# Optimization experiments

Hardware: AMD Instinct MI355X
Metric: run time of the kernel (lower is better)

The kernel has to match this reference:

```python
import jax, jax.numpy as jnp
import numpy as np

N_GRID = 16      # reservoir_n
CHANNELS = 4
R = 2            # receptive-field radius -> 5x5 kernel
T_STEPS = 8
NEG_SLOPE = 0.1


def _extract_patches(S):
    # S: [b, C, n, n] -> patches [b, C, 5, 5, n, n] (kernel offsets u,v)
    Sp = jnp.pad(S, ((0, 0), (0, 0), (R, R), (R, R)))
    k = 2 * R + 1
    rows = [jnp.stack([Sp[:, :, du:du + N_GRID, dv:dv + N_GRID] for dv in range(k)], axis=2)
            for du in range(k)]
    return jnp.stack(rows, axis=2)  # [b, C, k, k, n, n]


def _reservoir_step(S, W):
    # W: [n, n, C_out, C_in, k, k]; per-pixel unique weights (locally connected)
    patches = _extract_patches(S)                       # [b, c, u, v, y, x]
    out = jnp.einsum('bcuvyx,yxocuv->boyx', patches, W)  # [b, C, n, n]
    return jnp.where(out > 0, out, NEG_SLOPE * out)      # leaky_relu(0.1)


def setup_inputs() -> dict:
    key = jax.random.key(0)
    k1, k2 = jax.random.split(key)
    x = jax.random.normal(k1, (8192, 784), dtype=jnp.float32)
    # scale weights down so the T-step recurrence stays numerically tame
    W = jax.random.normal(k2, (N_GRID, N_GRID, CHANNELS, CHANNELS, 2 * R + 1, 2 * R + 1),
                          dtype=jnp.float32) * 0.05
    return {"x": x, "W": W}


def reference(x, W):
    batch = x.shape[0]
    total = N_GRID * N_GRID * CHANNELS  # 1024
    padded = jnp.pad(x, ((0, 0), (0, total - x.shape[1])))
    S = padded.reshape(batch, CHANNELS, N_GRID, N_GRID)
    for _ in range(T_STEPS):
        S = _reservoir_step(S, W)
    S_pooled = S.mean(axis=1)                 # pool over channels -> [b, n, n]
    return S_pooled.reshape(batch, -1)        # [b, n*n]
```

## Files before the change

### kernel.cpp

```cpp
#include <hip/hip_runtime.h>

#define NG 16
#define NC 4
#define BPB 8
#define TSTEPS 8
#define PITCH 34
#define CROW (NG * PITCH)

__device__ __forceinline__ void fma8(float w, const float4& s0, const float4& s1,
                                     float4& a0, float4& a1) {
    a0.x = fmaf(w, s0.x, a0.x);
    a0.y = fmaf(w, s0.y, a0.y);
    a0.z = fmaf(w, s0.z, a0.z);
    a0.w = fmaf(w, s0.w, a0.w);
    a1.x = fmaf(w, s1.x, a1.x);
    a1.y = fmaf(w, s1.y, a1.y);
    a1.z = fmaf(w, s1.z, a1.z);
    a1.w = fmaf(w, s1.w, a1.w);
}

__device__ __forceinline__ float4 lrelu4(float4 v) {
    float4 r;
    r.x = fmaxf(v.x, 0.1f * v.x);
    r.y = fmaxf(v.y, 0.1f * v.y);
    r.z = fmaxf(v.z, 0.1f * v.z);
    r.w = fmaxf(v.w, 0.1f * v.w);
    return r;
}

template<int CTRL>
__device__ __forceinline__ float dppf(float x) {
    return __int_as_float(__builtin_amdgcn_update_dpp(
        0, __float_as_int(x), CTRL, 0xF, 0xF, true));
}
template<int CTRL>
__device__ __forceinline__ float4 dpp4(float4 v) {
    float4 r;
    r.x = dppf<CTRL>(v.x);
    r.y = dppf<CTRL>(v.y);
    r.z = dppf<CTRL>(v.z);
    r.w = dppf<CTRL>(v.w);
    return r;
}

__global__ void wt_transpose(const float* __restrict__ W, float4* __restrict__ Wt) {
    int t = blockIdx.x * 256 + threadIdx.x;
    if (t >= 25600) return;
    int r = t >> 8;
    int pix = t & 255;
    int c = r / 25, uv = r - c * 25, u = uv / 5, v = uv - u * 5;
    int y = pix >> 4, x = pix & 15;
    float4 w = make_float4(0.f, 0.f, 0.f, 0.f);
    if ((unsigned)(y + u - 2) < 16u && (unsigned)(x + v - 2) < 16u) {
        int base = pix * 400 + c * 25 + uv;
        w.x = W[base];
        w.y = W[base + 100];
        w.z = W[base + 200];
        w.w = W[base + 300];
    }
    Wt[r * 256 + pix] = w;
}

__global__ __launch_bounds__(256, 4)
__attribute__((amdgpu_waves_per_eu(4, 4)))
void reservoir_kernel(const float* __restrict__ X, const float4* __restrict__ Wt,
                      float* __restrict__ out, int batch) {
    __shared__ float4 smv[NC * CROW];
    float* smf = reinterpret_cast<float*>(smv);

    const int tid = threadIdx.x;
    const int y = tid >> 4;
    const int x = tid & 15;
    const long itemBase = (long)blockIdx.x * BPB;

    const float4* Wp = Wt + tid;

    float4 b0_0, b0_1, b0_2, b0_3, b0_4;
    float4 b1_0, b1_1, b1_2, b1_3, b1_4;

#define LOADBUF(B, OFF) \
    B##_0 = Wp[(OFF)]; \
    B##_1 = Wp[(OFF) + 256]; \
    B##_2 = Wp[(OFF) + 512]; \
    B##_3 = Wp[(OFF) + 768]; \
    B##_4 = Wp[(OFF) + 1024];

    LOADBUF(b0, 0)

    for (int b = 0; b < BPB; ++b) {
        long item = itemBase + b;
        const float* xr = X + item * 784;
        const int g = b >> 2, j = b & 3;
        #pragma unroll
        for (int kk = 0; kk < 4; ++kk) {
            int idx = tid + kk * 256;
            float v = 0.f;
            if (idx < 784 && item < batch) v = __builtin_nontemporal_load(&xr[idx]);
            int c = idx >> 8, rem = idx & 255, yy = rem >> 4, xx = rem & 15;
            int phys = g ^ ((xx >> 2) & 1);
            smf[((c * NG + yy) * PITCH + xx * 2 + phys) * 4 + j] = v;
        }
    }

    int ybf[5];
    #pragma unroll
    for (int u = 0; u < 5; ++u) {
        int yy = y + u - 2;
        yy = yy < 0 ? 0 : (yy > 15 ? 15 : yy);
        ybf[u] = yy * PITCH;
    }
    const int swx = (x >> 2) & 1;
    const int xown = x * 2 + swx;
    const int pa = y * PITCH + x * 2;

    __syncthreads();

#define CHUNK_DPP(B, CB, U) { \
    const int i0 = (CB) + ybf[U] + xown; \
    const float4 s0 = smv[i0]; \
    const float4 s1 = smv[i0 ^ 1]; \
    fma8(B##_2.x, s0, s1, a00, a01); \
    fma8(B##_2.y, s0, s1, a10, a11); \
    fma8(B##_2.z, s0, s1, a20, a21); \
    fma8(B##_2.w, s0, s1, a30, a31); \
    { const float4 t0 = dpp4<0x111>(s0), t1 = dpp4<0x111>(s1); \
      fma8(B##_1.x, t0, t1, a00, a01); \
      fma8(B##_1.y, t0, t1, a10, a11); \
      fma8(B##_1.z, t0, t1, a20, a21); \
      fma8(B##_1.w, t0, t1, a30, a31); } \
    { const float4 t0 = dpp4<0x101>(s0), t1 = dpp4<0x101>(s1); \
      fma8(B##_3.x, t0, t1, a00, a01); \
      fma8(B##_3.y, t0, t1, a10, a11); \
      fma8(B##_3.z, t0, t1, a20, a21); \
      fma8(B##_3.w, t0, t1, a30, a31); } \
    { const float4 t0 = dpp4<0x112>(s0), t1 = dpp4<0x112>(s1); \
      fma8(B##_0.x, t0, t1, a00, a01); \
      fma8(B##_0.y, t0, t1, a10, a11); \
      fma8(B##_0.z, t0, t1, a20, a21); \
      fma8(B##_0.w, t0, t1, a30, a31); } \
    { const float4 t0 = dpp4<0x102>(s0), t1 = dpp4<0x102>(s1); \
      fma8(B##_4.x, t0, t1, a00, a01); \
      fma8(B##_4.y, t0, t1, a10, a11); \
      fma8(B##_4.z, t0, t1, a20, a21); \
      fma8(B##_4.w, t0, t1, a30, a31); } }

#define CH_A(CB, U, POFF) \
    LOADBUF(b1, POFF) \
    CHUNK_DPP(b0, CB, U)
#define CH_B(CB, U, POFF) \
    LOADBUF(b0, POFF) \
    CHUNK_DPP(b1, CB, U)

    #pragma unroll 1
    for (int t = 0; t < TSTEPS; ++t) {
        float4 a00 = {0,0,0,0}, a01 = {0,0,0,0};
        float4 a10 = {0,0,0,0}, a11 = {0,0,0,0};
        float4 a20 = {0,0,0,0}, a21 = {0,0,0,0};
        float4 a30 = {0,0,0,0}, a31 = {0,0,0,0};

        #pragma unroll 1
        for (int g = 0; g < 4; g += 2) {
            const int cb0 = g * CROW;
            const int cb1 = cb0 + CROW;
            const int wo = g * 6400;
            const int wlast = (g == 2) ? 0 : wo + 12800;

            CH_A(cb0, 0, wo + 1280)
            CH_B(cb0, 1, wo + 2560)
            CH_A(cb0, 2, wo + 3840)
            CH_B(cb0, 3, wo + 5120)
            CH_A(cb0, 4, wo + 6400)
            CH_B(cb1, 0, wo + 7680)
            CH_A(cb1, 1, wo + 8960)
            CH_B(cb1, 2, wo + 10240)
            CH_A(cb1, 3, wo + 11520)
            CH_B(cb1, 4, wlast)
        }

        a00 = lrelu4(a00); a01 = lrelu4(a01);
        a10 = lrelu4(a10); a11 = lrelu4(a11);
        a20 = lrelu4(a20); a21 = lrelu4(a21);
        a30 = lrelu4(a30); a31 = lrelu4(a31);

        if (t < TSTEPS - 1) {
            __syncthreads();
            int c0 = 0 * CROW + pa;
            smv[c0 + swx] = a00; smv[c0 + (swx ^ 1)] = a01;
            int c1 = 1 * CROW + pa;
            smv[c1 + swx] = a10; smv[c1 + (swx ^ 1)] = a11;
            int c2 = 2 * CROW + pa;
            smv[c2 + swx] = a20; smv[c2 + (swx ^ 1)] = a21;
            int c3 = 3 * CROW + pa;
            smv[c3 + swx] = a30; smv[c3 + (swx ^ 1)] = a31;
            __syncthreads();
        } else {
            float4 p0, p1;
            p0.x = (a00.x + a10.x + a20.x + a30.x) * 0.25f;
            p0.y = (a00.y + a10.y + a20.y + a30.y) * 0.25f;
            p0.z = (a00.z + a10.z + a20.z + a30.z) * 0.25f;
            p0.w = (a00.w + a10.w + a20.w + a30.w) * 0.25f;
            p1.x = (a01.x + a11.x + a21.x + a31.x) * 0.25f;
            p1.y = (a01.y + a11.y + a21.y + a31.y) * 0.25f;
            p1.z = (a01.z + a11.z + a21.z + a31.z) * 0.25f;
            p1.w = (a01.w + a11.w + a21.w + a31.w) * 0.25f;
            long ob = itemBase * 256 + tid;
            if (itemBase + 0 < batch) __builtin_nontemporal_store(p0.x, &out[ob + 0 * 256]);
            if (itemBase + 1 < batch) __builtin_nontemporal_store(p0.y, &out[ob + 1 * 256]);
            if (itemBase + 2 < batch) __builtin_nontemporal_store(p0.z, &out[ob + 2 * 256]);
            if (itemBase + 3 < batch) __builtin_nontemporal_store(p0.w, &out[ob + 3 * 256]);
            if (itemBase + 4 < batch) __builtin_nontemporal_store(p1.x, &out[ob + 4 * 256]);
            if (itemBase + 5 < batch) __builtin_nontemporal_store(p1.y, &out[ob + 5 * 256]);
            if (itemBase + 6 < batch) __builtin_nontemporal_store(p1.z, &out[ob + 6 * 256]);
            if (itemBase + 7 < batch) __builtin_nontemporal_store(p1.w, &out[ob + 7 * 256]);
        }
    }
}

extern "C" void kernel_launch(void* const* d_in, const int* in_sizes, int n_in,
                              void* d_out, int out_size, void* d_ws, size_t ws_size,
                              hipStream_t stream) {
    const float* X = (const float*)d_in[0];
    const float* W = (const float*)d_in[1];
    float* out = (float*)d_out;
    const int batch = in_sizes[0] / 784;
    const int blocks = (batch + BPB - 1) / BPB;

    wt_transpose<<<100, 256, 0, stream>>>(W, (float4*)d_ws);
    reservoir_kernel<<<blocks, 256, 0, stream>>>(
        X, (const float4*)d_ws, out, batch);
}
```

Baseline: 235.8 us.

## Split each block's eight items across two 256-thread halves with loop-based weight loads

Doubles the block to 512 threads so each thread owns 4 batch items instead of 8, halving accumulator registers and raising occupancy. The fully unrolled double-buffered weight pipeline is replaced with rolled c/u loops that load the next weight set after a sched barrier. In exchange, each weight is now loaded and reused by two threads, giving half the FMA work per weight load, and prefetch overlap is weaker.

Result: slower. 266.1 us (+12.8%).

```diff
diff --git a/kernel.cpp b/kernel.cpp
--- a/kernel.cpp
+++ b/kernel.cpp
@@ -7,16 +7,11 @@
 #define PITCH 34
 #define CROW (NG * PITCH)
 
-__device__ __forceinline__ void fma8(float w, const float4& s0, const float4& s1,
-                                     float4& a0, float4& a1) {
-    a0.x = fmaf(w, s0.x, a0.x);
-    a0.y = fmaf(w, s0.y, a0.y);
-    a0.z = fmaf(w, s0.z, a0.z);
-    a0.w = fmaf(w, s0.w, a0.w);
-    a1.x = fmaf(w, s1.x, a1.x);
-    a1.y = fmaf(w, s1.y, a1.y);
-    a1.z = fmaf(w, s1.z, a1.z);
-    a1.w = fmaf(w, s1.w, a1.w);
+__device__ __forceinline__ void fma4(float w, const float4& s, float4& a) {
+    a.x = fmaf(w, s.x, a.x);
+    a.y = fmaf(w, s.y, a.y);
+    a.z = fmaf(w, s.z, a.z);
+    a.w = fmaf(w, s.w, a.w);
 }
 
 __device__ __forceinline__ float4 lrelu4(float4 v) {
@@ -61,157 +56,103 @@
     Wt[r * 256 + pix] = w;
 }
 
-__global__ __launch_bounds__(256, 4)
-__attribute__((amdgpu_waves_per_eu(4, 4)))
+__global__ __launch_bounds__(512, 8)
 void reservoir_kernel(const float* __restrict__ X, const float4* __restrict__ Wt,
                       float* __restrict__ out, int batch) {
     __shared__ float4 smv[NC * CROW];
     float* smf = reinterpret_cast<float*>(smv);
 
     const int tid = threadIdx.x;
-    const int y = tid >> 4;
-    const int x = tid & 15;
+    const int bh  = tid >> 8;
+    const int pix = tid & 255;
+    const int y = pix >> 4;
+    const int x = pix & 15;
     const long itemBase = (long)blockIdx.x * BPB;
-
-    const float4* Wp = Wt + tid;
-
-    float4 b0_0, b0_1, b0_2, b0_3, b0_4;
-    float4 b1_0, b1_1, b1_2, b1_3, b1_4;
-
-#define LOADBUF(B, OFF) \
-    B##_0 = Wp[(OFF)]; \
-    B##_1 = Wp[(OFF) + 256]; \
-    B##_2 = Wp[(OFF) + 512]; \
-    B##_3 = Wp[(OFF) + 768]; \
-    B##_4 = Wp[(OFF) + 1024];
-
-    LOADBUF(b0, 0)
 
     for (int b = 0; b < BPB; ++b) {
         long item = itemBase + b;
-        const float* xr = X + item * 784;
-        const int g = b >> 2, j = b & 3;
         #pragma unroll
-        for (int kk = 0; kk < 4; ++kk) {
-            int idx = tid + kk * 256;
+        for (int k = 0; k < 2; ++k) {
+            int idx = tid + k * 512;
             float v = 0.f;
-            if (idx < 784 && item < batch) v = __builtin_nontemporal_load(&xr[idx]);
+            if (idx < 784 && item < batch)
+                v = __builtin_nontemporal_load(&X[item * 784 + idx]);
             int c = idx >> 8, rem = idx & 255, yy = rem >> 4, xx = rem & 15;
-            int phys = g ^ ((xx >> 2) & 1);
-            smf[((c * NG + yy) * PITCH + xx * 2 + phys) * 4 + j] = v;
+            int phys = (b >> 2) ^ ((xx >> 2) & 1);
+            smf[((c * NG + yy) * PITCH + xx * 2 + phys) * 4 + (b & 3)] = v;
         }
     }
 
-    int ybf[5];
-    #pragma unroll
-    for (int u = 0; u < 5; ++u) {
-        int yy = y + u - 2;
-        yy = yy < 0 ? 0 : (yy > 15 ? 15 : yy);
-        ybf[u] = yy * PITCH;
-    }
     const int swx = (x >> 2) & 1;
-    const int xown = x * 2 + swx;
-    const int pa = y * PITCH + x * 2;
+    const int xq  = x * 2 + (bh ^ swx);
+
+    const float4* Wp = Wt + pix;
+    float4 w0 = Wp[0], w1 = Wp[256], w2 = Wp[512], w3 = Wp[768], w4 = Wp[1024];
+    int wnext = 1280;
 
     __syncthreads();
 
-#define CHUNK_DPP(B, CB, U) { \
-    const int i0 = (CB) + ybf[U] + xown; \
-    const float4 s0 = smv[i0]; \
-    const float4 s1 = smv[i0 ^ 1]; \
-    fma8(B##_2.x, s0, s1, a00, a01); \
-    fma8(B##_2.y, s0, s1, a10, a11); \
-    fma8(B##_2.z, s0, s1, a20, a21); \
-    fma8(B##_2.w, s0, s1, a30, a31); \
-    { const float4 t0 = dpp4<0x111>(s0), t1 = dpp4<0x111>(s1); \
-      fma8(B##_1.x, t0, t1, a00, a01); \
-      fma8(B##_1.y, t0, t1, a10, a11); \
-      fma8(B##_1.z, t0, t1, a20, a21); \
-      fma8(B##_1.w, t0, t1, a30, a31); } \
-    { const float4 t0 = dpp4<0x101>(s0), t1 = dpp4<0x101>(s1); \
-      fma8(B##_3.x, t0, t1, a00, a01); \
-      fma8(B##_3.y, t0, t1, a10, a11); \
-      fma8(B##_3.z, t0, t1, a20, a21); \
-      fma8(B##_3.w, t0, t1, a30, a31); } \
-    { const float4 t0 = dpp4<0x112>(s0), t1 = dpp4<0x112>(s1); \
-      fma8(B##_0.x, t0, t1, a00, a01); \
-      fma8(B##_0.y, t0, t1, a10, a11); \
-      fma8(B##_0.z, t0, t1, a20, a21); \
-      fma8(B##_0.w, t0, t1, a30, a31); } \
-    { const float4 t0 = dpp4<0x102>(s0), t1 = dpp4<0x102>(s1); \
-      fma8(B##_4.x, t0, t1, a00, a01); \
-      fma8(B##_4.y, t0, t1, a10, a11); \
-      fma8(B##_4.z, t0, t1, a20, a21); \
-      fma8(B##_4.w, t0, t1, a30, a31); } }
-
-#define CH_A(CB, U, POFF) \
-    LOADBUF(b1, POFF) \
-    CHUNK_DPP(b0, CB, U)
-#define CH_B(CB, U, POFF) \
-    LOADBUF(b0, POFF) \
-    CHUNK_DPP(b1, CB, U)
-
     #pragma unroll 1
     for (int t = 0; t < TSTEPS; ++t) {
-        float4 a00 = {0,0,0,0}, a01 = {0,0,0,0};
-        float4 a10 = {0,0,0,0}, a11 = {0,0,0,0};
-        float4 a20 = {0,0,0,0}, a21 = {0,0,0,0};
-        float4 a30 = {0,0,0,0}, a31 = {0,0,0,0};
+        float4 a0 = {0,0,0,0}, a1 = {0,0,0,0}, a2 = {0,0,0,0}, a3 = {0,0,0,0};
 
         #pragma unroll 1
-        for (int g = 0; g < 4; g += 2) {
-            const int cb0 = g * CROW;
-            const int cb1 = cb0 + CROW;
-            const int wo = g * 6400;
-            const int wlast = (g == 2) ? 0 : wo + 12800;
+        for (int c = 0; c < NC; ++c) {
+            const int cb = c * CROW;
+            #pragma unroll 1
+            for (int u = 0; u < 5; ++u) {
+                int yy = y + u - 2;
+                yy = yy < 0 ? 0 : (yy > 15 ? 15 : yy);
+                const float4 s = smv[cb + yy * PITCH + xq];
 
-            CH_A(cb0, 0, wo + 1280)
-            CH_B(cb0, 1, wo + 2560)
-            CH_A(cb0, 2, wo + 3840)
-            CH_B(cb0, 3, wo + 5120)
-            CH_A(cb0, 4, wo + 6400)
-            CH_B(cb1, 0, wo + 7680)
-            CH_A(cb1, 1, wo + 8960)
-            CH_B(cb1, 2, wo + 10240)
-            CH_A(cb1, 3, wo + 11520)
-            CH_B(cb1, 4, wlast)
+                fma4(w2.x, s, a0); fma4(w2.y, s, a1);
+                fma4(w2.z, s, a2); fma4(w2.w, s, a3);
+                { const float4 tp = dpp4<0x111>(s);
+                  fma4(w1.x, tp, a0); fma4(w1.y, tp, a1);
+                  fma4(w1.z, tp, a2); fma4(w1.w, tp, a3); }
+                { const float4 tp = dpp4<0x101>(s);
+                  fma4(w3.x, tp, a0); fma4(w3.y, tp, a1);
+                  fma4(w3.z, tp, a2); fma4(w3.w, tp, a3); }
+                { const float4 tp = dpp4<0x112>(s);
+                  fma4(w0.x, tp, a0); fma4(w0.y, tp, a1);
+                  fma4(w0.z, tp, a2); fma4(w0.w, tp, a3); }
+                { const float4 tp = dpp4<0x102>(s);
+                  fma4(w4.x, tp, a0); fma4(w4.y, tp, a1);
+                  fma4(w4.z, tp, a2); fma4(w4.w, tp, a3); }
+
+                __builtin_amdgcn_sched_barrier(0);
+                w0 = Wp[wnext];
+                w1 = Wp[wnext + 256];
+                w2 = Wp[wnext + 512];
+                w3 = Wp[wnext + 768];
+                w4 = Wp[wnext + 1024];
+                wnext += 1280;
+                if (wnext >= 25600) wnext = 0;
+            }
         }
 
-        a00 = lrelu4(a00); a01 = lrelu4(a01);
-        a10 = lrelu4(a10); a11 = lrelu4(a11);
-        a20 = lrelu4(a20); a21 = lrelu4(a21);
-        a30 = lrelu4(a30); a31 = lrelu4(a31);
+        a0 = lrelu4(a0); a1 = lrelu4(a1); a2 = lrelu4(a2); a3 = lrelu4(a3);
 
         if (t < TSTEPS - 1) {
             __syncthreads();
-            int c0 = 0 * CROW + pa;
-            smv[c0 + swx] = a00; smv[c0 + (swx ^ 1)] = a01;
-            int c1 = 1 * CROW + pa;
-            smv[c1 + swx] = a10; smv[c1 + (swx ^ 1)] = a11;
-            int c2 = 2 * CROW + pa;
-            smv[c2 + swx] = a20; smv[c2 + (swx ^ 1)] = a21;
-            int c3 = 3 * CROW + pa;
-            smv[c3 + swx] = a30; smv[c3 + (swx ^ 1)] = a31;
+            const int pa = y * PITCH + x * 2 + (bh ^ swx);
+            smv[0 * CROW + pa] = a0;
+            smv[1 * CROW + pa] = a1;
+            smv[2 * CROW + pa] = a2;
+            smv[3 * CROW + pa] = a3;
             __syncthreads();
         } else {
-            float4 p0, p1;
-            p0.x = (a00.x + a10.x + a20.x + a30.x) * 0.25f;
-            p0.y = (a00.y + a10.y + a20.y + a30.y) * 0.25f;
-            p0.z = (a00.z + a10.z + a20.z + a30.z) * 0.25f;
-            p0.w = (a00.w + a10.w + a20.w + a30.w) * 0.25f;
-            p1.x = (a01.x + a11.x + a21.x + a31.x) * 0.25f;
-            p1.y = (a01.y + a11.y + a21.y + a31.y) * 0.25f;
-            p1.z = (a01.z + a11.z + a21.z + a31.z) * 0.25f;
-            p1.w = (a01.w + a11.w + a21.w + a31.w) * 0.25f;
-            long ob = itemBase * 256 + tid;
-            if (itemBase + 0 < batch) __builtin_nontemporal_store(p0.x, &out[ob + 0 * 256]);
-            if (itemBase + 1 < batch) __builtin_nontemporal_store(p0.y, &out[ob + 1 * 256]);
-            if (itemBase + 2 < batch) __builtin_nontemporal_store(p0.z, &out[ob + 2 * 256]);
-            if (itemBase + 3 < batch) __builtin_nontemporal_store(p0.w, &out[ob + 3 * 256]);
-            if (itemBase + 4 < batch) __builtin_nontemporal_store(p1.x, &out[ob + 4 * 256]);
-            if (itemBase + 5 < batch) __builtin_nontemporal_store(p1.y, &out[ob + 5 * 256]);
-            if (itemBase + 6 < batch) __builtin_nontemporal_store(p1.z, &out[ob + 6 * 256]);
-            if (itemBase + 7 < batch) __builtin_nontemporal_store(p1.w, &out[ob + 7 * 256]);
+            float4 p;
+            p.x = (a0.x + a1.x + a2.x + a3.x) * 0.25f;
+            p.y = (a0.y + a1.y + a2.y + a3.y) * 0.25f;
+            p.z = (a0.z + a1.z + a2.z + a3.z) * 0.25f;
+            p.w = (a0.w + a1.w + a2.w + a3.w) * 0.25f;
+            const long b0 = itemBase + bh * 4;
+            const long ob = b0 * 256 + pix;
+            if (b0 + 0 < batch) __builtin_nontemporal_store(p.x, &out[ob + 0 * 256]);
+            if (b0 + 1 < batch) __builtin_nontemporal_store(p.y, &out[ob + 1 * 256]);
+            if (b0 + 2 < batch) __builtin_nontemporal_store(p.z, &out[ob + 2 * 256]);
+            if (b0 + 3 < batch) __builtin_nontemporal_store(p.w, &out[ob + 3 * 256]);
         }
     }
 }
@@ -226,6 +167,6 @@
     const int blocks = (batch + BPB - 1) / BPB;
 
     wt_transpose<<<100, 256, 0, stream>>>(W, (float4*)d_ws);
-    reservoir_kernel<<<blocks, 256, 0, stream>>>(
+    reservoir_kernel<<<blocks, 512, 0, stream>>>(
         X, (const float4*)d_ws, out, batch);
 }
```
